# Optimization experiments

Measured on AMD Instinct MI355X. Metric: run time of the kernel, lower is better.

The kernel has to match this reference:

```python
import jax, jax.numpy as jnp
import numpy as np

B, S, HID = 2, 4096, 1024
NH, HD = 16, 64
R = 2  # dilation_rate


def setup_inputs() -> dict:
    key = jax.random.key(0)
    ks = jax.random.split(key, 6)
    sc = 0.02
    return {
        "hidden_states": jax.random.normal(ks[0], (B, S, HID), jnp.float32),
        "Wq": jax.random.normal(ks[1], (HID, HID), jnp.float32) * sc,
        "Wk": jax.random.normal(ks[2], (HID, HID), jnp.float32) * sc,
        "Wv": jax.random.normal(ks[3], (HID, HID), jnp.float32) * sc,
        "Wo": jax.random.normal(ks[4], (HID, HID), jnp.float32) * sc,
        "bo": jnp.zeros((HID,), jnp.float32),
    }


def reference(hidden_states, Wq, Wk, Wv, Wo, bo):
    bsz, q_len, _ = hidden_states.shape
    # projections (torch Linear: y = x @ W.T)
    q = jnp.einsum('bsh,oh->bso', hidden_states, Wq).reshape(bsz, q_len, NH, HD).transpose(0, 2, 1, 3)
    k = jnp.einsum('bsh,oh->bso', hidden_states, Wk).reshape(bsz, q_len, NH, HD).transpose(0, 2, 1, 3)
    v = jnp.einsum('bsh,oh->bso', hidden_states, Wv).reshape(bsz, q_len, NH, HD).transpose(0, 2, 1, 3)
    # strided dilation gather (indices 0, R, 2R, ...)
    q = q[:, :, ::R, :]
    k = k[:, :, ::R, :]
    v = v[:, :, ::R, :]
    sd = q.shape[2]  # dilated length
    # SDPA with is_causal=True over the dilated subsequence
    scores = jnp.einsum('bhqd,bhkd->bhqk', q, k) / np.sqrt(HD).astype(np.float32)
    causal = jnp.tril(jnp.ones((sd, sd), bool))
    scores = jnp.where(causal, scores, jnp.finfo(scores.dtype).min)
    probs = jax.nn.softmax(scores, axis=-1)
    attn = jnp.einsum('bhqk,bhkd->bhqd', probs, v)  # [B, H, sd, HD]
    attn = attn.transpose(0, 2, 1, 3).reshape(bsz, sd, HID)
    # scatter back into zero-initialized full-length tensor
    full = jnp.zeros((bsz, q_len, HID), attn.dtype).at[:, ::R, :].set(attn)
    return jnp.einsum('bsh,oh->bso', full, Wo) + bo
```

## Files before the change

### kernel.cpp

```cpp
#include <hip/hip_runtime.h>
#include <cstdint>

typedef unsigned short u16;
typedef unsigned int u32;
typedef __attribute__((ext_vector_type(8))) short short8;
typedef __attribute__((ext_vector_type(4))) float f32x4;
typedef __attribute__((ext_vector_type(4))) unsigned short u16x4;

#define S_ 4096
#define SD 2048

__device__ __forceinline__ u16 f2bf(float f) {
  union { float f; u32 u; } v; v.f = f;
  u32 r = v.u + 0x7fffu + ((v.u >> 16) & 1u);
  return (u16)(r >> 16);
}
#if __has_builtin(__builtin_amdgcn_cvt_pk_bf16_f32)
__device__ __forceinline__ u32 pkbf(float a, float b) {
  auto r = __builtin_amdgcn_cvt_pk_bf16_f32(a, b);
  u32 o; __builtin_memcpy(&o, &r, 4); return o;
}
#else
__device__ __forceinline__ u32 pkbf(float a, float b) {
  union { float f; u32 u; } ua, ub; ua.f = a; ub.f = b;
  return __builtin_amdgcn_perm(ub.u + 0x8000u, ua.u + 0x8000u, 0x07060302u);
}
#endif
__device__ __forceinline__ f32x4 mfma16(short8 a, short8 b, f32x4 c) {
  return __builtin_amdgcn_mfma_f32_16x16x32_bf16(a, b, c, 0, 0, 0);
}
__device__ __forceinline__ void async16(const void* g, void* l) {
  __builtin_amdgcn_global_load_lds((__attribute__((address_space(1))) void*)g,
                                   (__attribute__((address_space(3))) void*)l,
                                   16, 0, 0);
}

__global__ __launch_bounds__(256) void cast_all(const float* __restrict__ hs,
                                                const float* __restrict__ Wq,
                                                const float* __restrict__ Wk,
                                                const float* __restrict__ Wv,
                                                const float* __restrict__ Wo,
                                                u16* __restrict__ dstW,
                                                u16* __restrict__ dstX) {
  int bid = blockIdx.x;
  if (bid < 4096) {
    int gid = bid * 256 + threadIdx.x;
    int wsel = gid >> 18;
    int off  = (gid & 262143) * 4;
    const float* src = (wsel == 0) ? Wq : (wsel == 1) ? Wk : (wsel == 2) ? Wv : Wo;
    float scl = (wsel == 0) ? 0.18033688f : 1.0f;
    f32x4 v = *(const f32x4*)(src + off);
    u16x4 o; o.x = f2bf(v.x * scl); o.y = f2bf(v.y * scl);
    o.z = f2bf(v.z * scl); o.w = f2bf(v.w * scl);
    *(u16x4*)(dstW + (size_t)wsel * 1048576 + off) = o;
  } else {
    int gid = (bid - 4096) * 256 + threadIdx.x;
    int e = gid * 4;
    int m = e >> 10, col = e & 1023;
    int b = m >> 11, sm = m & 2047;
    const float* src = hs + ((size_t)(b * S_ + 2 * sm) << 10) + col;
    f32x4 v = *(const f32x4*)src;
    u16x4 o; o.x = f2bf(v.x); o.y = f2bf(v.y); o.z = f2bf(v.z); o.w = f2bf(v.w);
    *(u16x4*)(dstX + ((size_t)m << 10) + col) = o;
  }
}

__global__ __launch_bounds__(256) void qkv_gemm(const u16* __restrict__ X,
                                                const u16* __restrict__ Wbf,
                                                u16* __restrict__ QK,
                                                u16* __restrict__ Vt) {
  __shared__ __align__(16) char lA[16384];
  __shared__ __align__(16) char lB[8192];
  const int tid = threadIdx.x, lane = tid & 63, w = tid >> 6;
  const int quad = lane >> 4, l15 = lane & 15;
  int bid = blockIdx.x;
  const u16 *A, *B; u16* C; int N, bm, bn;
  if (bid < 1024) {
    A = X; B = Wbf; C = QK; N = 2048;
    bm = (bid >> 5) * 128; bn = (bid & 31) * 64;
  } else {
    int b2 = bid - 1024;
    A = Wbf + 2 * 1048576; B = X; C = Vt; N = 4096;
    bm = (b2 >> 6) * 128; bn = (b2 & 63) * 64;
  }
  const int wm = (w & 1) * 64, wn = (w >> 1) * 32;
  f32x4 acc[4][2] = {};

  auto stage = [&](int buf, int k0) {
#pragma unroll
    for (int i = 0; i < 2; i++) {
      int p = i * 256 + tid;
      int row = p >> 2, cp = p & 3;
      int c = cp ^ ((row ^ (row >> 2)) & 3);
      async16(A + (size_t)(bm + row) * 1024 + k0 + c * 8,
              lA + buf * 8192 + i * 4096 + w * 1024);
    }
    {
      int p = tid;
      int row = p >> 2, cp = p & 3;
      int c = cp ^ ((row ^ (row >> 2)) & 3);
      async16(B + (size_t)(bn + row) * 1024 + k0 + c * 8,
              lB + buf * 4096 + w * 1024);
    }
  };

  stage(0, 0);
#pragma unroll 1
  for (int kt = 0; kt < 32; kt++) {
    __syncthreads();
    if (kt + 1 < 32) stage((kt + 1) & 1, (kt + 1) * 32);
    const char* A_ = lA + (kt & 1) * 8192;
    const char* B_ = lB + (kt & 1) * 4096;
    short8 af[4], bf[2];
#pragma unroll
    for (int mi = 0; mi < 4; mi++) {
      int row = wm + mi * 16 + l15;
      af[mi] = *(const short8*)(A_ + (row * 4 + (quad ^ ((row ^ (row >> 2)) & 3))) * 16);
    }
#pragma unroll
    for (int ni = 0; ni < 2; ni++) {
      int row = wn + ni * 16 + l15;
      bf[ni] = *(const short8*)(B_ + (row * 4 + (quad ^ ((row ^ (row >> 2)) & 3))) * 16);
    }
#pragma unroll
    for (int mi = 0; mi < 4; mi++)
#pragma unroll
      for (int ni = 0; ni < 2; ni++)
        acc[mi][ni] = mfma16(af[mi], bf[ni], acc[mi][ni]);
  }
#pragma unroll
  for (int mi = 0; mi < 4; mi++)
#pragma unroll
    for (int ni = 0; ni < 2; ni++) {
      int m0 = bm + wm + mi * 16 + quad * 4;
      int n = bn + wn + ni * 16 + l15;
#pragma unroll
      for (int r = 0; r < 4; r++)
        C[(size_t)(m0 + r) * N + n] = f2bf(acc[mi][ni][r]);
    }
}

__global__ __launch_bounds__(256) void oproj(const u16* __restrict__ A,
                                             const u16* __restrict__ B,
                                             const float* __restrict__ bo,
                                             float* __restrict__ out) {
  __shared__ __align__(16) char lA[8192];
  __shared__ __align__(16) char lB[8192];
  const int tid = threadIdx.x, lane = tid & 63, w = tid >> 6;
  const int quad = lane >> 4, l15 = lane & 15;
  const int bm = blockIdx.y * 64, bn = blockIdx.x * 64;
  const int wm = (w & 1) * 32, wn = (w >> 1) * 32;
  f32x4 acc[2][2] = {};

  auto stage = [&](int buf, int k0) {
    int row = tid >> 2, cp = tid & 3;
    int c = cp ^ ((row ^ (row >> 2)) & 3);
    async16(A + (size_t)(bm + row) * 1024 + k0 + c * 8, lA + buf * 4096 + w * 1024);
    async16(B + (size_t)(bn + row) * 1024 + k0 + c * 8, lB + buf * 4096 + w * 1024);
  };

  stage(0, 0);
#pragma unroll 1
  for (int kt = 0; kt < 32; kt++) {
    __syncthreads();
    if (kt + 1 < 32) stage((kt + 1) & 1, (kt + 1) * 32);
    const char* A_ = lA + (kt & 1) * 4096;
    const char* B_ = lB + (kt & 1) * 4096;
    short8 af[2], bf[2];
#pragma unroll
    for (int mi = 0; mi < 2; mi++) {
      int row = wm + mi * 16 + l15;
      af[mi] = *(const short8*)(A_ + (row * 4 + (quad ^ ((row ^ (row >> 2)) & 3))) * 16);
    }
#pragma unroll
    for (int ni = 0; ni < 2; ni++) {
      int row = wn + ni * 16 + l15;
      bf[ni] = *(const short8*)(B_ + (row * 4 + (quad ^ ((row ^ (row >> 2)) & 3))) * 16);
    }
#pragma unroll
    for (int mi = 0; mi < 2; mi++)
#pragma unroll
      for (int ni = 0; ni < 2; ni++)
        acc[mi][ni] = mfma16(af[mi], bf[ni], acc[mi][ni]);
  }
#pragma unroll
  for (int mi = 0; mi < 2; mi++)
#pragma unroll
    for (int ni = 0; ni < 2; ni++) {
      int n = bn + wn + ni * 16 + l15;
      float bias = bo[n];
#pragma unroll
      for (int r = 0; r < 4; r++) {
        int m = bm + wm + mi * 16 + quad * 4 + r;
        int bb = m >> 11, sm = m & 2047;
        size_t grow = ((size_t)(bb * S_ + 2 * sm)) << 10;
        out[grow + n] = acc[mi][ni][r] + bias;
        out[grow + 1024 + n] = bias;
      }
    }
}

__global__ __launch_bounds__(256) void attn4(const u16* __restrict__ QK,
                                             const u16* __restrict__ Vt,
                                             u16* __restrict__ O) {
  __shared__ __align__(16) char lK[2][8192];
  __shared__ __align__(16) char lP[4][2048];
  const int tid = threadIdx.x, lane = tid & 63, w = tid >> 6;
  const int quad = lane >> 4, l15 = lane & 15;
  const int h = blockIdx.x, b = blockIdx.y;
  const int qt = 31 - (int)blockIdx.z;
  const int qb = qt * 64 + w * 16;
  const int sw = l15 & 7;

  const u16* qp = QK + (size_t)(b * SD + qb + l15) * 2048 + h * 64 + quad * 8;
  short8 qf0 = *(const short8*)qp;
  short8 qf1 = *(const short8*)(qp + 32);

  auto stageK = [&](int buf, int kb) {
#pragma unroll
    for (int i = 0; i < 2; i++) {
      int p = (w * 2 + i) * 64 + lane;
      int row = p >> 3, c = (p & 7) ^ (row & 7);
      async16(QK + (size_t)(b * SD + kb + row) * 2048 + 1024 + h * 64 + c * 8,
              lK[buf] + (w * 2 + i) * 1024);
    }
  };

  f32x4 oacc[4] = {};
  float l4[4] = {0.f, 0.f, 0.f, 0.f};
  char* Pw = lP[w];
  const u16* vbase = Vt + ((size_t)(h * 64 + l15)) * 4096 + b * SD + quad * 8;

  stageK(0, 0);
#pragma unroll 1
  for (int kt = 0; kt <= qt; kt++) {
    const int kb = kt * 64;
    __syncthreads();
    short8 vf0[4], vf1[4];
#pragma unroll
    for (int m = 0; m < 4; m++) {
      const u16* vp = vbase + (size_t)(m * 16) * 4096 + kb;
      vf0[m] = *(const short8*)vp;
      vf1[m] = *(const short8*)(vp + 32);
    }
    if (kt + 1 <= qt) stageK((kt + 1) & 1, (kt + 1) * 64);
    const char* K_ = lK[kt & 1];

    f32x4 s[4];
#pragma unroll
    for (int m = 0; m < 4; m++) {
      int key = m * 16 + l15;
      short8 kf0 = *(const short8*)(K_ + (key * 8 + (quad ^ (key & 7))) * 16);
      short8 kf1 = *(const short8*)(K_ + (key * 8 + ((4 + quad) ^ (key & 7))) * 16);
      f32x4 a = {};
      a = mfma16(kf0, qf0, a);
      a = mfma16(kf1, qf1, a);
      s[m] = a;
    }
    if (kt == qt) {
      int qrel = w * 16 + l15;
#pragma unroll
      for (int m = 0; m < 4; m++)
#pragma unroll
        for (int r = 0; r < 4; r++)
          if (m * 16 + quad * 4 + r > qrel) s[m][r] = -1e30f;
    }
    float pr[4][4];
#pragma unroll
    for (int m = 0; m < 4; m++) {
#pragma unroll
      for (int r = 0; r < 4; r++) pr[m][r] = exp2f(s[m][r]);
      l4[m] += (pr[m][0] + pr[m][1]) + (pr[m][2] + pr[m][3]);
    }
#pragma unroll
    for (int m = 0; m < 4; m++) {
      int c = m * 2 + (quad >> 1);
      int base = l15 * 128 + ((c ^ sw) * 16) + (quad & 1) * 8;
      *(u32*)(Pw + base)     = pkbf(pr[m][0], pr[m][1]);
      *(u32*)(Pw + base + 4) = pkbf(pr[m][2], pr[m][3]);
    }
    short8 pf0 = *(const short8*)(Pw + l15 * 128 + ((quad ^ sw) * 16));
    short8 pf1 = *(const short8*)(Pw + l15 * 128 + (((4 + quad) ^ sw) * 16));

#pragma unroll
    for (int m = 0; m < 4; m++) {
      oacc[m] = mfma16(vf0[m], pf0, oacc[m]);
      oacc[m] = mfma16(vf1[m], pf1, oacc[m]);
    }
  }
  float l = (l4[0] + l4[1]) + (l4[2] + l4[3]);
  l += __shfl_xor(l, 16, 64);
  l += __shfl_xor(l, 32, 64);
  float inv = 1.0f / l;
  u16* op = O + (size_t)(b * SD + qb + l15) * 1024 + h * 64;
#pragma unroll
  for (int m = 0; m < 4; m++) {
    u16x4 ov;
#pragma unroll
    for (int r = 0; r < 4; r++) ov[r] = f2bf(oacc[m][r] * inv);
    *(u16x4*)(op + m * 16 + quad * 4) = ov;
  }
}

extern "C" void kernel_launch(void* const* d_in, const int* in_sizes, int n_in,
                              void* d_out, int out_size, void* d_ws, size_t ws_size,
                              hipStream_t stream) {
  (void)in_sizes; (void)n_in; (void)out_size; (void)ws_size;
  const float* hs = (const float*)d_in[0];
  const float* Wq = (const float*)d_in[1];
  const float* Wk = (const float*)d_in[2];
  const float* Wv = (const float*)d_in[3];
  const float* Wo = (const float*)d_in[4];
  const float* bo = (const float*)d_in[5];
  float* out = (float*)d_out;
  char* ws = (char*)d_ws;

  u16* Xbf = (u16*)ws;
  u16* Wbf = (u16*)(ws + (8u << 20));
  u16* QKb = (u16*)(ws + (16u << 20));
  u16* Vtb = (u16*)(ws + (32u << 20));
  u16* Ob  = (u16*)(ws + (40u << 20));

  cast_all<<<8192, 256, 0, stream>>>(hs, Wq, Wk, Wv, Wo, Wbf, Xbf);
  qkv_gemm<<<1536, 256, 0, stream>>>(Xbf, Wbf, QKb, Vtb);
  attn4<<<dim3(16, 2, 32), 256, 0, stream>>>(QKb, Vtb, Ob);
  oproj<<<dim3(16, 64), 256, 0, stream>>>(Ob, Wbf + 3 * 1048576, bo, out);
}
```

Before: 229.6 us.

## Enlarge GEMM tiles and double-buffer V fragments in attention loop

The QKV GEMM tile grows from 128x64 to 128x256 and the output projection tile from 64x64 to 64x128, so each block reuses its A tile across more columns and loads less from global memory overall. The attention kernel now prefetches the next V tile into a second register set while computing the current one, hiding global load latency. In exchange, the QKV grid shrinks to 384 blocks on a GPU with many CUs, which may leave units idle. Accumulator and fragment register counts also rise a lot, which could reduce occupancy or cause spills.

After: 256.6 us. +11.7%, slower.

```diff
diff --git a/kernel.cpp b/kernel.cpp
--- a/kernel.cpp
+++ b/kernel.cpp
@@ -70,21 +70,21 @@
                                                 u16* __restrict__ QK,
                                                 u16* __restrict__ Vt) {
   __shared__ __align__(16) char lA[16384];
-  __shared__ __align__(16) char lB[8192];
+  __shared__ __align__(16) char lB[32768];
   const int tid = threadIdx.x, lane = tid & 63, w = tid >> 6;
   const int quad = lane >> 4, l15 = lane & 15;
   int bid = blockIdx.x;
   const u16 *A, *B; u16* C; int N, bm, bn;
-  if (bid < 1024) {
+  if (bid < 256) {
     A = X; B = Wbf; C = QK; N = 2048;
-    bm = (bid >> 5) * 128; bn = (bid & 31) * 64;
+    bm = (bid >> 3) * 128; bn = (bid & 7) * 256;
   } else {
-    int b2 = bid - 1024;
+    int b2 = bid - 256;
     A = Wbf + 2 * 1048576; B = X; C = Vt; N = 4096;
-    bm = (b2 >> 6) * 128; bn = (b2 & 63) * 64;
-  }
-  const int wm = (w & 1) * 64, wn = (w >> 1) * 32;
-  f32x4 acc[4][2] = {};
+    bm = (b2 >> 4) * 128; bn = (b2 & 15) * 256;
+  }
+  const int wm = (w & 1) * 64, wn = (w >> 1) * 128;
+  f32x4 acc[4][8] = {};
 
   auto stage = [&](int buf, int k0) {
 #pragma unroll
@@ -95,12 +95,13 @@
       async16(A + (size_t)(bm + row) * 1024 + k0 + c * 8,
               lA + buf * 8192 + i * 4096 + w * 1024);
     }
-    {
-      int p = tid;
+#pragma unroll
+    for (int i = 0; i < 4; i++) {
+      int p = i * 256 + tid;
       int row = p >> 2, cp = p & 3;
       int c = cp ^ ((row ^ (row >> 2)) & 3);
       async16(B + (size_t)(bn + row) * 1024 + k0 + c * 8,
-              lB + buf * 4096 + w * 1024);
+              lB + buf * 16384 + i * 4096 + w * 1024);
     }
   };
 
@@ -110,28 +111,28 @@
     __syncthreads();
     if (kt + 1 < 32) stage((kt + 1) & 1, (kt + 1) * 32);
     const char* A_ = lA + (kt & 1) * 8192;
-    const char* B_ = lB + (kt & 1) * 4096;
-    short8 af[4], bf[2];
+    const char* B_ = lB + (kt & 1) * 16384;
+    short8 af[4], bf[8];
 #pragma unroll
     for (int mi = 0; mi < 4; mi++) {
       int row = wm + mi * 16 + l15;
       af[mi] = *(const short8*)(A_ + (row * 4 + (quad ^ ((row ^ (row >> 2)) & 3))) * 16);
     }
 #pragma unroll
-    for (int ni = 0; ni < 2; ni++) {
+    for (int ni = 0; ni < 8; ni++) {
       int row = wn + ni * 16 + l15;
       bf[ni] = *(const short8*)(B_ + (row * 4 + (quad ^ ((row ^ (row >> 2)) & 3))) * 16);
     }
 #pragma unroll
     for (int mi = 0; mi < 4; mi++)
 #pragma unroll
-      for (int ni = 0; ni < 2; ni++)
+      for (int ni = 0; ni < 8; ni++)
         acc[mi][ni] = mfma16(af[mi], bf[ni], acc[mi][ni]);
   }
 #pragma unroll
   for (int mi = 0; mi < 4; mi++)
 #pragma unroll
-    for (int ni = 0; ni < 2; ni++) {
+    for (int ni = 0; ni < 8; ni++) {
       int m0 = bm + wm + mi * 16 + quad * 4;
       int n = bn + wn + ni * 16 + l15;
 #pragma unroll
@@ -145,18 +146,26 @@
                                              const float* __restrict__ bo,
                                              float* __restrict__ out) {
   __shared__ __align__(16) char lA[8192];
-  __shared__ __align__(16) char lB[8192];
+  __shared__ __align__(16) char lB[16384];
   const int tid = threadIdx.x, lane = tid & 63, w = tid >> 6;
   const int quad = lane >> 4, l15 = lane & 15;
-  const int bm = blockIdx.y * 64, bn = blockIdx.x * 64;
-  const int wm = (w & 1) * 32, wn = (w >> 1) * 32;
-  f32x4 acc[2][2] = {};
+  const int bm = blockIdx.y * 64, bn = blockIdx.x * 128;
+  const int wm = (w & 1) * 32, wn = (w >> 1) * 64;
+  f32x4 acc[2][4] = {};
 
   auto stage = [&](int buf, int k0) {
-    int row = tid >> 2, cp = tid & 3;
-    int c = cp ^ ((row ^ (row >> 2)) & 3);
-    async16(A + (size_t)(bm + row) * 1024 + k0 + c * 8, lA + buf * 4096 + w * 1024);
-    async16(B + (size_t)(bn + row) * 1024 + k0 + c * 8, lB + buf * 4096 + w * 1024);
+    {
+      int row = tid >> 2, cp = tid & 3;
+      int c = cp ^ ((row ^ (row >> 2)) & 3);
+      async16(A + (size_t)(bm + row) * 1024 + k0 + c * 8, lA + buf * 4096 + w * 1024);
+    }
+#pragma unroll
+    for (int i = 0; i < 2; i++) {
+      int p = i * 256 + tid;
+      int row = p >> 2, cp = p & 3;
+      int c = cp ^ ((row ^ (row >> 2)) & 3);
+      async16(B + (size_t)(bn + row) * 1024 + k0 + c * 8, lB + buf * 8192 + i * 4096 + w * 1024);
+    }
   };
 
   stage(0, 0);
@@ -165,28 +174,28 @@
     __syncthreads();
     if (kt + 1 < 32) stage((kt + 1) & 1, (kt + 1) * 32);
     const char* A_ = lA + (kt & 1) * 4096;
-    const char* B_ = lB + (kt & 1) * 4096;
-    short8 af[2], bf[2];
+    const char* B_ = lB + (kt & 1) * 8192;
+    short8 af[2], bf[4];
 #pragma unroll
     for (int mi = 0; mi < 2; mi++) {
       int row = wm + mi * 16 + l15;
       af[mi] = *(const short8*)(A_ + (row * 4 + (quad ^ ((row ^ (row >> 2)) & 3))) * 16);
     }
 #pragma unroll
-    for (int ni = 0; ni < 2; ni++) {
+    for (int ni = 0; ni < 4; ni++) {
       int row = wn + ni * 16 + l15;
       bf[ni] = *(const short8*)(B_ + (row * 4 + (quad ^ ((row ^ (row >> 2)) & 3))) * 16);
     }
 #pragma unroll
     for (int mi = 0; mi < 2; mi++)
 #pragma unroll
-      for (int ni = 0; ni < 2; ni++)
+      for (int ni = 0; ni < 4; ni++)
         acc[mi][ni] = mfma16(af[mi], bf[ni], acc[mi][ni]);
   }
 #pragma unroll
   for (int mi = 0; mi < 2; mi++)
 #pragma unroll
-    for (int ni = 0; ni < 2; ni++) {
+    for (int ni = 0; ni < 4; ni++) {
       int n = bn + wn + ni * 16 + l15;
       float bias = bo[n];
 #pragma unroll
@@ -200,7 +209,7 @@
     }
 }
 
-__global__ __launch_bounds__(256) void attn4(const u16* __restrict__ QK,
+__global__ __launch_bounds__(256) void attn5(const u16* __restrict__ QK,
                                              const u16* __restrict__ Vt,
                                              u16* __restrict__ O) {
   __shared__ __align__(16) char lK[2][8192];
@@ -226,24 +235,30 @@
     }
   };
 
+  const u16* vbase = Vt + ((size_t)(h * 64 + l15)) * 4096 + b * SD + quad * 8;
+  auto ldV = [&](int kb, short8* v0, short8* v1) {
+#pragma unroll
+    for (int m = 0; m < 4; m++) {
+      const u16* vp = vbase + (size_t)(m * 16) * 4096 + kb;
+      v0[m] = *(const short8*)vp;
+      v1[m] = *(const short8*)(vp + 32);
+    }
+  };
+
   f32x4 oacc[4] = {};
   float l4[4] = {0.f, 0.f, 0.f, 0.f};
   char* Pw = lP[w];
-  const u16* vbase = Vt + ((size_t)(h * 64 + l15)) * 4096 + b * SD + quad * 8;
+  short8 va0[4], va1[4], vb0[4], vb1[4];
 
   stageK(0, 0);
-#pragma unroll 1
-  for (int kt = 0; kt <= qt; kt++) {
-    const int kb = kt * 64;
+  ldV(0, va0, va1);
+
+  auto body = [&](int kt, short8* v0, short8* v1, short8* n0, short8* n1) {
     __syncthreads();
-    short8 vf0[4], vf1[4];
-#pragma unroll
-    for (int m = 0; m < 4; m++) {
-      const u16* vp = vbase + (size_t)(m * 16) * 4096 + kb;
-      vf0[m] = *(const short8*)vp;
-      vf1[m] = *(const short8*)(vp + 32);
-    }
-    if (kt + 1 <= qt) stageK((kt + 1) & 1, (kt + 1) * 64);
+    if (kt + 1 <= qt) {
+      stageK((kt + 1) & 1, (kt + 1) * 64);
+      ldV((kt + 1) * 64, n0, n1);
+    }
     const char* K_ = lK[kt & 1];
 
     f32x4 s[4];
@@ -284,10 +299,17 @@
 
 #pragma unroll
     for (int m = 0; m < 4; m++) {
-      oacc[m] = mfma16(vf0[m], pf0, oacc[m]);
-      oacc[m] = mfma16(vf1[m], pf1, oacc[m]);
-    }
-  }
+      oacc[m] = mfma16(v0[m], pf0, oacc[m]);
+      oacc[m] = mfma16(v1[m], pf1, oacc[m]);
+    }
+  };
+
+#pragma unroll 1
+  for (int kt = 0; kt <= qt; kt += 2) {
+    body(kt, va0, va1, vb0, vb1);
+    if (kt + 1 <= qt) body(kt + 1, vb0, vb1, va0, va1);
+  }
+
   float l = (l4[0] + l4[1]) + (l4[2] + l4[3]);
   l += __shfl_xor(l, 16, 64);
   l += __shfl_xor(l, 32, 64);
@@ -322,7 +344,7 @@
   u16* Ob  = (u16*)(ws + (40u << 20));
 
   cast_all<<<8192, 256, 0, stream>>>(hs, Wq, Wk, Wv, Wo, Wbf, Xbf);
-  qkv_gemm<<<1536, 256, 0, stream>>>(Xbf, Wbf, QKb, Vtb);
-  attn4<<<dim3(16, 2, 32), 256, 0, stream>>>(QKb, Vtb, Ob);
-  oproj<<<dim3(16, 64), 256, 0, stream>>>(Ob, Wbf + 3 * 1048576, bo, out);
-}
+  qkv_gemm<<<384, 256, 0, stream>>>(Xbf, Wbf, QKb, Vtb);
+  attn5<<<dim3(16, 2, 32), 256, 0, stream>>>(QKb, Vtb, Ob);
+  oproj<<<dim3(8, 64), 256, 0, stream>>>(Ob, Wbf + 3 * 1048576, bo, out);
+}
```
